# Performance work log

Measured on AMD Instinct MI355X. Metric: run time of the kernel, lower is better.

Reference implementation:

```python
import jax, jax.numpy as jnp
import numpy as np
import math

B, S, DIM, H, HD = 2, 2048, 2048, 16, 128


def _rotary(t, cos, sin):
    # t: [B, S, H, HD]; cos/sin: [S, HD//2]
    tr = t.reshape(*t.shape[:-1], HD // 2, 2)
    t_re, t_im = tr[..., 0], tr[..., 1]
    c = cos[None, :, None, :]
    s = sin[None, :, None, :]
    o_re = t_re * c - t_im * s
    o_im = t_re * s + t_im * c
    out = jnp.stack([o_re, o_im], axis=-1)
    return out.reshape(t.shape)


def setup_inputs() -> dict:
    key = jax.random.key(0)
    ks = jax.random.split(key, 6)
    x = jax.random.normal(ks[0], (B, S, DIM), dtype=jnp.float32)
    # rotary frequencies (base 10000), matching complex freqs_cis = exp(i * t * freq)
    inv_freq = 1.0 / (10000.0 ** (np.arange(0, HD, 2, dtype=np.float32) / HD))
    t = np.arange(S, dtype=np.float32)
    ang = np.outer(t, inv_freq)  # [S, HD//2]
    freqs_cos = jnp.asarray(np.cos(ang), dtype=jnp.float32)
    freqs_sin = jnp.asarray(np.sin(ang), dtype=jnp.float32)
    # causal boolean mask [1,1,S,S]
    mask = jnp.tril(jnp.ones((S, S), dtype=bool))[None, None]
    scale = 0.02
    qw = jax.random.normal(ks[1], (DIM, H * HD), dtype=jnp.float32) * scale
    kw = jax.random.normal(ks[2], (DIM, H * HD), dtype=jnp.float32) * scale
    vw = jax.random.normal(ks[3], (DIM, H * HD), dtype=jnp.float32) * scale
    ow = jax.random.normal(ks[4], (H * HD, DIM), dtype=jnp.float32) * scale
    return {"x": x, "freqs_cos": freqs_cos, "freqs_sin": freqs_sin, "mask": mask,
            "qw": qw, "kw": kw, "vw": vw, "ow": ow}


def reference(x, freqs_cos, freqs_sin, mask, qw, kw, vw, ow):
    bsz, slen, _ = x.shape
    q = (x @ qw).reshape(bsz, slen, H, HD)
    k = (x @ kw).reshape(bsz, slen, H, HD)
    v = (x @ vw).reshape(bsz, slen, H, HD)
    q = _rotary(q, freqs_cos[:slen], freqs_sin[:slen])
    k = _rotary(k, freqs_cos[:slen], freqs_sin[:slen])
    # [B, H, S, HD]
    q = q.transpose(0, 2, 1, 3)
    k = k.transpose(0, 2, 1, 3)
    v = v.transpose(0, 2, 1, 3)
    scale = 1.0 / math.sqrt(HD)
    scores = jnp.einsum('bhqd,bhkd->bhqk', q, k) * scale
    neg_inf = jnp.finfo(scores.dtype).min
    scores = jnp.where(mask, scores, neg_inf)
    attn_w = jax.nn.softmax(scores, axis=-1)
    attn = jnp.einsum('bhqk,bhkd->bhqd', attn_w, v)
    attn = attn.transpose(0, 2, 1, 3).reshape(bsz, slen, H * HD)
    out = attn @ ow
    return (out, attn_w)
```

## Files before the change

kernel.cpp:

```cpp
#include <hip/hip_runtime.h>
#include <stdint.h>

#define S 2048
#define DIMM 2048
#define NH 16
#define HD 128
#define NB 2
#define M4 4096

typedef unsigned short u16;
typedef unsigned int u32;
typedef __attribute__((ext_vector_type(8))) short short8;
typedef __attribute__((ext_vector_type(4))) float f32x4;

__device__ __forceinline__ u16 f2bf(float f) {
  union { float f; u32 u; } v; v.f = f;
  u32 u = v.u + 0x7fffu + ((v.u >> 16) & 1u);
  return (u16)(u >> 16);
}
__device__ __forceinline__ float bf2f(u16 b) {
  union { u32 u; float f; } v; v.u = ((u32)b) << 16;
  return v.f;
}
__device__ __forceinline__ u32 cvt_pk_bf16(float lo, float hi) {
  u32 r; asm("v_cvt_pk_bf16_f32 %0, %1, %2" : "=v"(r) : "v"(lo), "v"(hi)); return r;
}
__device__ __forceinline__ void gl_lds16(const void* g, void* l) {
  __builtin_amdgcn_global_load_lds((const __attribute__((address_space(1))) void*)g,
                                   (__attribute__((address_space(3))) void*)l, 16, 0, 0);
}

__global__ __launch_bounds__(256) void k_conv_x(const float* __restrict__ x, u16* __restrict__ xb) {
  int i = (blockIdx.x * 256 + threadIdx.x) * 8;
  float4 a = *(const float4*)&x[i];
  float4 b = *(const float4*)&x[i + 4];
  uint4 o;
  o.x = (u32)f2bf(a.x) | ((u32)f2bf(a.y) << 16);
  o.y = (u32)f2bf(a.z) | ((u32)f2bf(a.w) << 16);
  o.z = (u32)f2bf(b.x) | ((u32)f2bf(b.y) << 16);
  o.w = (u32)f2bf(b.z) | ((u32)f2bf(b.w) << 16);
  *(uint4*)&xb[i] = o;
}

__global__ __launch_bounds__(256) void k_transpose_w4(const float* __restrict__ w0, const float* __restrict__ w1,
                                                      const float* __restrict__ w2, const float* __restrict__ w3,
                                                      u16* __restrict__ t0, u16* __restrict__ t1,
                                                      u16* __restrict__ t2, u16* __restrict__ t3) {
  __shared__ u16 t[64][72];
  int zi = blockIdx.z;
  const float* w = (zi == 0) ? w0 : (zi == 1) ? w1 : (zi == 2) ? w2 : w3;
  u16* wt = (zi == 0) ? t0 : (zi == 1) ? t1 : (zi == 2) ? t2 : t3;
  int k0 = blockIdx.y * 64, n0 = blockIdx.x * 64;
  int tid = threadIdx.x;
  int r0 = tid >> 4, c4 = (tid & 15) * 4;
#pragma unroll
  for (int p = 0; p < 4; ++p) {
    int r = r0 + p * 16;
    float4 v = *(const float4*)&w[(size_t)(k0 + r) * DIMM + n0 + c4];
    t[c4 + 0][r] = f2bf(v.x); t[c4 + 1][r] = f2bf(v.y);
    t[c4 + 2][r] = f2bf(v.z); t[c4 + 3][r] = f2bf(v.w);
  }
  __syncthreads();
#pragma unroll
  for (int p = 0; p < 2; ++p) {
    int cc = tid + p * 256;
    int rn = cc >> 3, ck = (cc & 7) * 8;
    *(uint4*)&wt[(size_t)(n0 + rn) * DIMM + k0 + ck] = *(const uint4*)&t[rn][ck];
  }
}

__device__ __forceinline__ void gemm128_core(const u16* __restrict__ A, const u16* __restrict__ Bt,
                                             int m0, int n0, int Kd, u16* lA, u16* lB,
                                             f32x4 acc[4][4]) {
  int tid = threadIdx.x;
  int lane = tid & 63;
  int wid = tid >> 6;
  int wm = wid >> 1, wn = wid & 1;
  int c0 = tid, c1 = tid + 256;
  int a_r0 = c0 >> 2, a_k0 = (c0 & 3) * 8;
  int a_r1 = c1 >> 2, a_k1 = (c1 & 3) * 8;
  int ln = lane & 15, sub = lane >> 4;
  for (int kt = 0; kt < Kd; kt += 32) {
    gl_lds16(&A[(size_t)(m0 + a_r0) * Kd + kt + a_k0], &lA[c0 * 8]);
    gl_lds16(&A[(size_t)(m0 + a_r1) * Kd + kt + a_k1], &lA[c1 * 8]);
    gl_lds16(&Bt[(size_t)(n0 + a_r0) * Kd + kt + a_k0], &lB[c0 * 8]);
    gl_lds16(&Bt[(size_t)(n0 + a_r1) * Kd + kt + a_k1], &lB[c1 * 8]);
    __syncthreads();
    short8 af[4], bf[4];
#pragma unroll
    for (int mf = 0; mf < 4; ++mf)
      af[mf] = *(const short8*)&lA[(wm * 64 + mf * 16 + ln) * 32 + sub * 8];
#pragma unroll
    for (int nf = 0; nf < 4; ++nf)
      bf[nf] = *(const short8*)&lB[(wn * 64 + nf * 16 + ln) * 32 + sub * 8];
#pragma unroll
    for (int mf = 0; mf < 4; ++mf)
#pragma unroll
      for (int nf = 0; nf < 4; ++nf)
        acc[mf][nf] = __builtin_amdgcn_mfma_f32_16x16x32_bf16(af[mf], bf[nf], acc[mf][nf], 0, 0, 0);
    __syncthreads();
  }
}

__global__ __launch_bounds__(256) void k_gemm_qkv(const u16* __restrict__ xb,
                                                  const u16* __restrict__ qwT, const u16* __restrict__ kwT,
                                                  const u16* __restrict__ vwT,
                                                  const float* __restrict__ fc, const float* __restrict__ fs,
                                                  u16* __restrict__ qws, u16* __restrict__ kws,
                                                  u16* __restrict__ vtws, float* __restrict__ aw_all) {
  __shared__ u16 lA[128 * 32], lB[128 * 32];
  int f = blockIdx.y * 48 + blockIdx.x;
  int fp = (f & 7) * 192 + (f >> 3);
  int bx = fp % 48, byy = fp / 48;

  {
    int tid = threadIdx.x;
    f32x4 zf = {0.f, 0.f, 0.f, 0.f};
#pragma unroll
    for (int z = 0; z < 5; ++z) {
      int t = f * 5 + z;
      int head = t / 240;
      int r = t - head * 240;
      int qt = 15;
#pragma unroll
      for (int q = 15; q >= 1; --q) {
        if (r >= q * (31 - q)) { qt = q; break; }
        if (q == 1) qt = 0;
      }
      int j = r - qt * (31 - qt);
      int kt = 2 * qt + 2 + j;
      float* base = aw_all + (size_t)head * S * S + (size_t)(qt * 128) * S + kt * 64;
#pragma unroll
      for (int i = 0; i < 8; ++i) {
        int c = i * 256 + tid;
        int row = c >> 4, col = (c & 15) * 4;
        __builtin_nontemporal_store(zf, (f32x4*)&base[(size_t)row * S + col]);
      }
    }
  }

  int region = bx >> 4;
  const u16* Bt = (region == 0) ? qwT : ((region == 1) ? kwT : vwT);
  int n0 = (bx & 15) * 128;
  int m0 = byy * 128;
  f32x4 acc[4][4];
  f32x4 z4 = {0.f, 0.f, 0.f, 0.f};
#pragma unroll
  for (int i = 0; i < 4; ++i)
#pragma unroll
    for (int j = 0; j < 4; ++j) acc[i][j] = z4;
  gemm128_core(xb, Bt, m0, n0, DIMM, lA, lB, acc);
  int lane = threadIdx.x & 63, wid = threadIdx.x >> 6;
  int wm = wid >> 1, wn = wid & 1;
  int ln = lane & 15, sub = lane >> 4;
  if (region == 2) {
#pragma unroll
    for (int mf = 0; mf < 4; ++mf)
#pragma unroll
      for (int nf = 0; nf < 4; ++nf) {
        int m = m0 + wm * 64 + mf * 16 + sub * 4;
        int nl = n0 + wn * 64 + nf * 16 + ln;
        int b = m >> 11, s = m & 2047;
        int h = nl >> 7, d = nl & 127;
        u32 w0 = cvt_pk_bf16(acc[mf][nf][0], acc[mf][nf][1]);
        u32 w1 = cvt_pk_bf16(acc[mf][nf][2], acc[mf][nf][3]);
        uint2 pw = {w0, w1};
        *(uint2*)&vtws[((size_t)((b << 4) + h) * HD + d) * S + s] = pw;
      }
  } else {
    u16* dst = (region == 0) ? qws : kws;
#pragma unroll
    for (int mf = 0; mf < 4; ++mf)
#pragma unroll
      for (int nf = 0; nf < 4; ++nf) {
        int mbase = m0 + wm * 64 + mf * 16 + sub * 4;
        int nl = n0 + wn * 64 + nf * 16 + ln;
        int h = nl >> 7, d = nl & 127;
        int pi = d >> 1;
#pragma unroll
        for (int r = 0; r < 4; ++r) {
          int m = mbase + r;
          int b = m >> 11, s = m & 2047;
          float c = fc[s * 64 + pi];
          float sn = fs[s * 64 + pi];
          float v = acc[mf][nf][r];
          float prt = __shfl_xor(v, 1);
          float o = (ln & 1) ? (prt * sn + v * c) : (v * c - prt * sn);
          float o2 = __shfl_xor(o, 1);
          if (!(ln & 1)) {
            u32 opk = cvt_pk_bf16(o, o2);
            *(u32*)&dst[((size_t)((b << 4) + h) * S + s) * HD + d] = opk;
          }
        }
      }
  }
}

__global__ __launch_bounds__(512, 4) void k_attn(const u16* __restrict__ qws, const u16* __restrict__ kws,
                                                 const u16* __restrict__ vtws,
                                                 float* __restrict__ aw_all, u16* __restrict__ att) {
  __shared__ u16 lK[2][64 * 128];
  __shared__ u16 lV[2][128 * 64];
  __shared__ u16 lP[128 * 64];

  int f = blockIdx.y * 16 + blockIdx.x;
  int x = f & 7;
  int j = f >> 3;
  int by = 4 * x + (j & 3);
  int u = j >> 2;
  int qt = (u < 8) ? u : 23 - u;
  int b = by >> 4, h = by & 15;
  const u16* qb = qws + (size_t)by * S * HD;
  const u16* kb = kws + (size_t)by * S * HD;
  const u16* vb = vtws + (size_t)by * HD * S;
  float* aw = aw_all + (size_t)by * S * S;
  int tid = threadIdx.x, lane = tid & 63, w = tid >> 6;
  int sub = lane >> 4, ln = lane & 15;
  int l7 = ln & 7;
  int q0 = qt * 128;
  int qrow = w * 16 + ln;
  int nkt = 2 * qt + 2;
  const float SC = 0.08838834764831845f * 1.4426950408889634f;

  auto stageK = [&](int kt, int bs) {
#pragma unroll
    for (int i = 0; i < 2; ++i) {
      int c = tid + i * 512;
      int row = c >> 4, p = c & 15;
      gl_lds16(&kb[(size_t)(kt * 64 + row) * HD + ((p ^ (row & 7)) << 3)], &lK[bs][c * 8]);
    }
  };
  auto stageV = [&](int kt, int bs) {
#pragma unroll
    for (int i = 0; i < 2; ++i) {
      int c = tid + i * 512;
      int row = c >> 3, p = c & 7;
      gl_lds16(&vb[(size_t)row * S + kt * 64 + ((p ^ (row & 7)) << 3)], &lV[bs][c * 8]);
    }
  };

  u16* lVlin = &lV[0][0];
#pragma unroll
  for (int i = 0; i < 4; ++i) {
    int c = tid + i * 512;
    int row = c >> 4, p = c & 15;
    gl_lds16(&qb[(size_t)(q0 + row) * HD + ((p ^ (row & 7)) << 3)], &lVlin[c * 8]);
  }
  stageK(0, 0);
  __syncthreads();

  short8 qf[4];
#pragma unroll
  for (int ks = 0; ks < 4; ++ks)
    qf[ks] = *(const short8*)&lVlin[qrow * 128 + (((ks * 4 + sub) ^ l7) << 3)];

  float ts = 0.f;
  for (int kt = 0; kt < nkt; ++kt) {
    int cur = kt & 1;
    if (kt + 1 < nkt) stageK(kt + 1, cur ^ 1);
    f32x4 sacc[4];
    f32x4 z4 = {0.f, 0.f, 0.f, 0.f};
#pragma unroll
    for (int nf = 0; nf < 4; ++nf) sacc[nf] = z4;
    __builtin_amdgcn_s_setprio(1);
#pragma unroll
    for (int nf = 0; nf < 4; ++nf) {
      int krow = nf * 16 + ln;
#pragma unroll
      for (int ks = 0; ks < 4; ++ks) {
        short8 kf = *(const short8*)&lK[cur][krow * 128 + (((ks * 4 + sub) ^ l7) << 3)];
        sacc[nf] = __builtin_amdgcn_mfma_f32_16x16x32_bf16(kf, qf[ks], sacc[nf], 0, 0, 0);
      }
    }
    __builtin_amdgcn_s_setprio(0);
    bool msk = (kt >= 2 * qt);
#pragma unroll
    for (int nf = 0; nf < 4; ++nf)
#pragma unroll
      for (int r = 0; r < 4; ++r) {
        float zz = sacc[nf][r] * SC;
        bool dead = msk && (kt * 64 + nf * 16 + sub * 4 + r > q0 + qrow);
        if (!dead) ts += exp2f(zz);
      }
    __syncthreads();
  }
  ts += __shfl_xor(ts, 16);
  ts += __shfl_xor(ts, 32);
  float mb = __log2f(ts);

  f32x4 oacc[8];
  {
    f32x4 z4 = {0.f, 0.f, 0.f, 0.f};
#pragma unroll
    for (int i = 0; i < 8; ++i) oacc[i] = z4;
  }
  stageK(nkt - 1, 0);
  stageV(nkt - 1, 0);
  __syncthreads();
  for (int it = 0; it < nkt; ++it) {
    int kt = nkt - 1 - it;
    int cur = it & 1;
    if (it + 1 < nkt) { stageK(kt - 1, cur ^ 1); stageV(kt - 1, cur ^ 1); }
    f32x4 sacc[4];
    f32x4 z4 = {0.f, 0.f, 0.f, 0.f};
#pragma unroll
    for (int nf = 0; nf < 4; ++nf) sacc[nf] = z4;
    __builtin_amdgcn_s_setprio(1);
#pragma unroll
    for (int nf = 0; nf < 4; ++nf) {
      int krow = nf * 16 + ln;
#pragma unroll
      for (int ks = 0; ks < 4; ++ks) {
        short8 kf = *(const short8*)&lK[cur][krow * 128 + (((ks * 4 + sub) ^ l7) << 3)];
        sacc[nf] = __builtin_amdgcn_mfma_f32_16x16x32_bf16(kf, qf[ks], sacc[nf], 0, 0, 0);
      }
    }
    __builtin_amdgcn_s_setprio(0);
    bool msk = (kt >= 2 * qt);
#pragma unroll
    for (int nf = 0; nf < 4; ++nf) {
      float p0 = exp2f(sacc[nf][0] * SC - mb);
      float p1 = exp2f(sacc[nf][1] * SC - mb);
      float p2 = exp2f(sacc[nf][2] * SC - mb);
      float p3 = exp2f(sacc[nf][3] * SC - mb);
      if (msk) {
        int base = kt * 64 + nf * 16 + sub * 4 - (q0 + qrow);
        if (base + 0 > 0) p0 = 0.f;
        if (base + 1 > 0) p1 = 0.f;
        if (base + 2 > 0) p2 = 0.f;
        if (base + 3 > 0) p3 = 0.f;
      }
      f32x4 pv = {p0, p1, p2, p3};
      __builtin_nontemporal_store(pv, (f32x4*)&aw[(size_t)(q0 + qrow) * S + kt * 64 + nf * 16 + sub * 4]);
      u32 w0 = cvt_pk_bf16(p0, p1);
      u32 w1 = cvt_pk_bf16(p2, p3);
      uint2 pw = {w0, w1};
      *(uint2*)&lP[qrow * 64 + (((nf * 2 + (sub >> 1)) ^ l7) << 3) + ((sub & 1) << 2)] = pw;
    }
    short8 pa[2];
#pragma unroll
    for (int ks2 = 0; ks2 < 2; ++ks2)
      pa[ks2] = *(const short8*)&lP[qrow * 64 + (((ks2 * 4 + sub) ^ l7) << 3)];
    __builtin_amdgcn_s_setprio(1);
#pragma unroll
    for (int nf2 = 0; nf2 < 8; ++nf2) {
      int drow = nf2 * 16 + ln;
#pragma unroll
      for (int ks2 = 0; ks2 < 2; ++ks2) {
        short8 vv = *(const short8*)&lV[cur][drow * 64 + (((ks2 * 4 + sub) ^ l7) << 3)];
        oacc[nf2] = __builtin_amdgcn_mfma_f32_16x16x32_bf16(vv, pa[ks2], oacc[nf2], 0, 0, 0);
      }
    }
    __builtin_amdgcn_s_setprio(0);
    __syncthreads();
  }

#pragma unroll
  for (int nf2 = 0; nf2 < 8; ++nf2) {
    u32 w0 = cvt_pk_bf16(oacc[nf2][0], oacc[nf2][1]);
    u32 w1 = cvt_pk_bf16(oacc[nf2][2], oacc[nf2][3]);
    uint2 ow2 = {w0, w1};
    *(uint2*)&att[(size_t)(b * S + q0 + qrow) * (NH * HD) + h * 128 + nf2 * 16 + sub * 4] = ow2;
  }
}

__global__ __launch_bounds__(256) void k_gemm_out(const u16* __restrict__ att, const u16* __restrict__ owT,
                                                  float* __restrict__ out) {
  __shared__ u16 lA[128 * 32], lB[128 * 32];
  int f = blockIdx.y * 16 + blockIdx.x;
  int fp = (f & 7) * 64 + (f >> 3);
  int n0 = (fp & 15) * 128, m0 = (fp >> 4) * 128;
  f32x4 acc[4][4];
  f32x4 z4 = {0.f, 0.f, 0.f, 0.f};
#pragma unroll
  for (int i = 0; i < 4; ++i)
#pragma unroll
    for (int j = 0; j < 4; ++j) acc[i][j] = z4;
  gemm128_core(att, owT, m0, n0, DIMM, lA, lB, acc);
  int lane = threadIdx.x & 63, wid = threadIdx.x >> 6;
  int wm = wid >> 1, wn = wid & 1;
  int ln = lane & 15, sub = lane >> 4;
#pragma unroll
  for (int mf = 0; mf < 4; ++mf)
#pragma unroll
    for (int nf = 0; nf < 4; ++nf)
#pragma unroll
      for (int r = 0; r < 4; ++r) {
        int m = m0 + wm * 64 + mf * 16 + sub * 4 + r;
        int nl = n0 + wn * 64 + nf * 16 + ln;
        out[(size_t)m * DIMM + nl] = acc[mf][nf][r];
      }
}

extern "C" void kernel_launch(void* const* d_in, const int* in_sizes, int n_in,
                              void* d_out, int out_size, void* d_ws, size_t ws_size,
                              hipStream_t stream) {
  const float* x  = (const float*)d_in[0];
  const float* fc = (const float*)d_in[1];
  const float* fs = (const float*)d_in[2];
  const float* qw = (const float*)d_in[4];
  const float* kw = (const float*)d_in[5];
  const float* vw = (const float*)d_in[6];
  const float* ow = (const float*)d_in[7];
  float* out = (float*)d_out;
  float* aw  = out + (size_t)M4 * DIMM;

  char* wsb = (char*)d_ws;
  u16* xb   = (u16*)(wsb);
  u16* qwT  = (u16*)(wsb + (size_t)16 * 1024 * 1024);
  u16* kwT  = (u16*)(wsb + (size_t)24 * 1024 * 1024);
  u16* vwT  = (u16*)(wsb + (size_t)32 * 1024 * 1024);
  u16* owT  = (u16*)(wsb + (size_t)40 * 1024 * 1024);
  u16* qws  = (u16*)(wsb + (size_t)48 * 1024 * 1024);
  u16* kws  = (u16*)(wsb + (size_t)64 * 1024 * 1024);
  u16* vtws = (u16*)(wsb + (size_t)80 * 1024 * 1024);
  u16* att  = (u16*)(wsb + (size_t)96 * 1024 * 1024);

  k_conv_x<<<4096, 256, 0, stream>>>(x, xb);
  k_transpose_w4<<<dim3(32, 32, 4), 256, 0, stream>>>(qw, kw, vw, ow, qwT, kwT, vwT, owT);
  k_gemm_qkv<<<dim3(48, 32), 256, 0, stream>>>(xb, qwT, kwT, vwT, fc, fs, qws, kws, vtws, aw);
  k_attn<<<dim3(16, 32), 512, 0, stream>>>(qws, kws, vtws, aw, att);
  k_gemm_out<<<dim3(16, 32), 256, 0, stream>>>(att, owT, out);
}
```

Measured before the change: 419.3 us.

## Rewrite QKV GEMM as 256x256 tile, 8-wave kernel with double-buffered LDS

Replaces the 128x128, 4-wave QKV projection GEMM with a 256x256-tile, 512-thread kernel (384 blocks). K-step is 64, LDS is double-buffered with XOR swizzle, and async global-to-LDS prefetch of the next K-tile is interleaved with MFMA phases using explicit waitcnt and barriers. The aim is more data reuse per LDS load and overlapping memory with compute. It costs heavy register pressure (128 accumulator floats per thread), 128KB of LDS, and a more fragile hand-scheduled sync scheme. Zero-filling of the masked attention weights is redistributed to match the new grid.

```diff
diff --git a/kernel.cpp b/kernel.cpp
--- a/kernel.cpp
+++ b/kernel.cpp
@@ -29,6 +29,7 @@
   __builtin_amdgcn_global_load_lds((const __attribute__((address_space(1))) void*)g,
                                    (__attribute__((address_space(3))) void*)l, 16, 0, 0);
 }
+#define MFMA16(a, b, c) __builtin_amdgcn_mfma_f32_16x16x32_bf16(a, b, c, 0, 0, 0)
 
 __global__ __launch_bounds__(256) void k_conv_x(const float* __restrict__ x, u16* __restrict__ xb) {
   int i = (blockIdx.x * 256 + threadIdx.x) * 8;
@@ -97,28 +98,28 @@
     for (int mf = 0; mf < 4; ++mf)
 #pragma unroll
       for (int nf = 0; nf < 4; ++nf)
-        acc[mf][nf] = __builtin_amdgcn_mfma_f32_16x16x32_bf16(af[mf], bf[nf], acc[mf][nf], 0, 0, 0);
+        acc[mf][nf] = MFMA16(af[mf], bf[nf], acc[mf][nf]);
     __syncthreads();
   }
 }
 
-__global__ __launch_bounds__(256) void k_gemm_qkv(const u16* __restrict__ xb,
-                                                  const u16* __restrict__ qwT, const u16* __restrict__ kwT,
-                                                  const u16* __restrict__ vwT,
-                                                  const float* __restrict__ fc, const float* __restrict__ fs,
-                                                  u16* __restrict__ qws, u16* __restrict__ kws,
-                                                  u16* __restrict__ vtws, float* __restrict__ aw_all) {
-  __shared__ u16 lA[128 * 32], lB[128 * 32];
-  int f = blockIdx.y * 48 + blockIdx.x;
-  int fp = (f & 7) * 192 + (f >> 3);
-  int bx = fp % 48, byy = fp / 48;
+__global__ __launch_bounds__(512, 2) void k_gemm_qkv8(const u16* __restrict__ xb,
+                                                      const u16* __restrict__ qwT, const u16* __restrict__ kwT,
+                                                      const u16* __restrict__ vwT,
+                                                      const float* __restrict__ fc, const float* __restrict__ fs,
+                                                      u16* __restrict__ qws, u16* __restrict__ kws,
+                                                      u16* __restrict__ vtws, float* __restrict__ aw_all) {
+  __shared__ u16 sm[2][2][256 * 64];
+  int tid = threadIdx.x;
+  int f = blockIdx.x;
+  int fp = (f & 7) * 48 + (f >> 3);
+  int bx = fp % 24, by = fp / 24;
 
   {
-    int tid = threadIdx.x;
     f32x4 zf = {0.f, 0.f, 0.f, 0.f};
 #pragma unroll
-    for (int z = 0; z < 5; ++z) {
-      int t = f * 5 + z;
+    for (int z = 0; z < 20; ++z) {
+      int t = f * 20 + z;
       int head = t / 240;
       int r = t - head * 240;
       int qt = 15;
@@ -131,35 +132,150 @@
       int kt = 2 * qt + 2 + j;
       float* base = aw_all + (size_t)head * S * S + (size_t)(qt * 128) * S + kt * 64;
 #pragma unroll
-      for (int i = 0; i < 8; ++i) {
-        int c = i * 256 + tid;
+      for (int i = 0; i < 4; ++i) {
+        int c = i * 512 + tid;
         int row = c >> 4, col = (c & 15) * 4;
         __builtin_nontemporal_store(zf, (f32x4*)&base[(size_t)row * S + col]);
       }
     }
   }
 
-  int region = bx >> 4;
+  int region = bx >> 3;
   const u16* Bt = (region == 0) ? qwT : ((region == 1) ? kwT : vwT);
-  int n0 = (bx & 15) * 128;
-  int m0 = byy * 128;
-  f32x4 acc[4][4];
+  int n0g = (bx & 7) * 256;
+  int m0g = by * 256;
+
+  int lane = tid & 63, wid = tid >> 6;
+  int wm = wid >> 2, wn = wid & 3;
+  int ln = lane & 15, sub = lane >> 4;
+
+  auto stagePart = [&](int t, int bs, int part) {
+    int mat = part >> 1, r0 = (part & 1) << 7;
+    const u16* src = mat ? Bt : xb;
+    int rb = (mat ? n0g : m0g) + r0;
+    int kk = t << 6;
+#pragma unroll
+    for (int i = 0; i < 2; ++i) {
+      int c = tid + i * 512;
+      int row = c >> 3, p = c & 7;
+      gl_lds16(&src[(size_t)(rb + row) * DIMM + kk + ((p ^ (row & 7)) << 3)],
+               &sm[bs][mat][((r0 + row) << 6) + (p << 3)]);
+    }
+  };
+  auto rdA = [&](int bs, int mf, int ks) -> short8 {
+    int row = (wm << 7) + (mf << 4) + ln;
+    return *(const short8*)&sm[bs][0][(row << 6) + ((((ks << 2) + sub) ^ (row & 7)) << 3)];
+  };
+  auto rdB = [&](int bs, int nf, int ks) -> short8 {
+    int row = (wn << 6) + (nf << 4) + ln;
+    return *(const short8*)&sm[bs][1][(row << 6) + ((((ks << 2) + sub) ^ (row & 7)) << 3)];
+  };
+
+  f32x4 acc[8][4];
   f32x4 z4 = {0.f, 0.f, 0.f, 0.f};
 #pragma unroll
-  for (int i = 0; i < 4; ++i)
+  for (int i = 0; i < 8; ++i)
 #pragma unroll
     for (int j = 0; j < 4; ++j) acc[i][j] = z4;
-  gemm128_core(xb, Bt, m0, n0, DIMM, lA, lB, acc);
-  int lane = threadIdx.x & 63, wid = threadIdx.x >> 6;
-  int wm = wid >> 1, wn = wid & 1;
-  int ln = lane & 15, sub = lane >> 4;
+
+  stagePart(0, 0, 0); stagePart(0, 0, 1); stagePart(0, 0, 2); stagePart(0, 0, 3);
+  __syncthreads();
+
+  const int nt = DIMM / 64;
+  for (int t = 0; t < nt; ++t) {
+    int cur = t & 1, nb = cur ^ 1;
+    bool pf = (t + 1 < nt);
+    short8 bfr[4][2];
+    if (pf) { stagePart(t + 1, nb, 0); stagePart(t + 1, nb, 1); }
+    asm volatile("s_waitcnt vmcnt(4)" ::: "memory");
+    __builtin_amdgcn_s_barrier();
+    __builtin_amdgcn_sched_barrier(0);
+#pragma unroll
+    for (int nf = 0; nf < 4; ++nf)
+#pragma unroll
+      for (int ks = 0; ks < 2; ++ks) bfr[nf][ks] = rdB(cur, nf, ks);
+    {
+      short8 a00 = rdA(cur, 0, 0), a01 = rdA(cur, 0, 1);
+      short8 a10 = rdA(cur, 1, 0), a11 = rdA(cur, 1, 1);
+      asm volatile("s_waitcnt lgkmcnt(0)" ::: "memory");
+      __builtin_amdgcn_sched_barrier(0);
+      __builtin_amdgcn_s_setprio(1);
+#pragma unroll
+      for (int nf = 0; nf < 4; ++nf) {
+        acc[0][nf] = MFMA16(a00, bfr[nf][0], acc[0][nf]);
+        acc[0][nf] = MFMA16(a01, bfr[nf][1], acc[0][nf]);
+        acc[1][nf] = MFMA16(a10, bfr[nf][0], acc[1][nf]);
+        acc[1][nf] = MFMA16(a11, bfr[nf][1], acc[1][nf]);
+      }
+      __builtin_amdgcn_s_setprio(0);
+    }
+    __builtin_amdgcn_s_barrier();
+    __builtin_amdgcn_sched_barrier(0);
+    {
+      short8 a00 = rdA(cur, 2, 0), a01 = rdA(cur, 2, 1);
+      short8 a10 = rdA(cur, 3, 0), a11 = rdA(cur, 3, 1);
+      if (pf) { stagePart(t + 1, nb, 2); stagePart(t + 1, nb, 3); }
+      __builtin_amdgcn_s_barrier();
+      asm volatile("s_waitcnt lgkmcnt(0)" ::: "memory");
+      __builtin_amdgcn_sched_barrier(0);
+      __builtin_amdgcn_s_setprio(1);
+#pragma unroll
+      for (int nf = 0; nf < 4; ++nf) {
+        acc[2][nf] = MFMA16(a00, bfr[nf][0], acc[2][nf]);
+        acc[2][nf] = MFMA16(a01, bfr[nf][1], acc[2][nf]);
+        acc[3][nf] = MFMA16(a10, bfr[nf][0], acc[3][nf]);
+        acc[3][nf] = MFMA16(a11, bfr[nf][1], acc[3][nf]);
+      }
+      __builtin_amdgcn_s_setprio(0);
+    }
+    __builtin_amdgcn_s_barrier();
+    __builtin_amdgcn_sched_barrier(0);
+    {
+      short8 a00 = rdA(cur, 4, 0), a01 = rdA(cur, 4, 1);
+      short8 a10 = rdA(cur, 5, 0), a11 = rdA(cur, 5, 1);
+      __builtin_amdgcn_s_barrier();
+      asm volatile("s_waitcnt lgkmcnt(0)" ::: "memory");
+      __builtin_amdgcn_sched_barrier(0);
+      __builtin_amdgcn_s_setprio(1);
+#pragma unroll
+      for (int nf = 0; nf < 4; ++nf) {
+        acc[4][nf] = MFMA16(a00, bfr[nf][0], acc[4][nf]);
+        acc[4][nf] = MFMA16(a01, bfr[nf][1], acc[4][nf]);
+        acc[5][nf] = MFMA16(a10, bfr[nf][0], acc[5][nf]);
+        acc[5][nf] = MFMA16(a11, bfr[nf][1], acc[5][nf]);
+      }
+      __builtin_amdgcn_s_setprio(0);
+    }
+    __builtin_amdgcn_s_barrier();
+    __builtin_amdgcn_sched_barrier(0);
+    {
+      short8 a00 = rdA(cur, 6, 0), a01 = rdA(cur, 6, 1);
+      short8 a10 = rdA(cur, 7, 0), a11 = rdA(cur, 7, 1);
+      __builtin_amdgcn_s_barrier();
+      asm volatile("s_waitcnt lgkmcnt(0)" ::: "memory");
+      __builtin_amdgcn_sched_barrier(0);
+      __builtin_amdgcn_s_setprio(1);
+#pragma unroll
+      for (int nf = 0; nf < 4; ++nf) {
+        acc[6][nf] = MFMA16(a00, bfr[nf][0], acc[6][nf]);
+        acc[6][nf] = MFMA16(a01, bfr[nf][1], acc[6][nf]);
+        acc[7][nf] = MFMA16(a10, bfr[nf][0], acc[7][nf]);
+        acc[7][nf] = MFMA16(a11, bfr[nf][1], acc[7][nf]);
+      }
+      __builtin_amdgcn_s_setprio(0);
+    }
+    asm volatile("s_waitcnt lgkmcnt(0)" ::: "memory");
+    __builtin_amdgcn_s_barrier();
+    __builtin_amdgcn_sched_barrier(0);
+  }
+
   if (region == 2) {
 #pragma unroll
-    for (int mf = 0; mf < 4; ++mf)
+    for (int mf = 0; mf < 8; ++mf)
 #pragma unroll
       for (int nf = 0; nf < 4; ++nf) {
-        int m = m0 + wm * 64 + mf * 16 + sub * 4;
-        int nl = n0 + wn * 64 + nf * 16 + ln;
+        int m = m0g + wm * 128 + mf * 16 + sub * 4;
+        int nl = (bx & 7) * 256 + wn * 64 + nf * 16 + ln;
         int b = m >> 11, s = m & 2047;
         int h = nl >> 7, d = nl & 127;
         u32 w0 = cvt_pk_bf16(acc[mf][nf][0], acc[mf][nf][1]);
@@ -170,11 +286,11 @@
   } else {
     u16* dst = (region == 0) ? qws : kws;
 #pragma unroll
-    for (int mf = 0; mf < 4; ++mf)
+    for (int mf = 0; mf < 8; ++mf)
 #pragma unroll
       for (int nf = 0; nf < 4; ++nf) {
-        int mbase = m0 + wm * 64 + mf * 16 + sub * 4;
-        int nl = n0 + wn * 64 + nf * 16 + ln;
+        int mbase = m0g + wm * 128 + mf * 16 + sub * 4;
+        int nl = (bx & 7) * 256 + wn * 64 + nf * 16 + ln;
         int h = nl >> 7, d = nl & 127;
         int pi = d >> 1;
 #pragma unroll
@@ -269,7 +385,7 @@
 #pragma unroll
       for (int ks = 0; ks < 4; ++ks) {
         short8 kf = *(const short8*)&lK[cur][krow * 128 + (((ks * 4 + sub) ^ l7) << 3)];
-        sacc[nf] = __builtin_amdgcn_mfma_f32_16x16x32_bf16(kf, qf[ks], sacc[nf], 0, 0, 0);
+        sacc[nf] = MFMA16(kf, qf[ks], sacc[nf]);
       }
     }
     __builtin_amdgcn_s_setprio(0);
@@ -289,11 +405,8 @@
   float mb = __log2f(ts);
 
   f32x4 oacc[8];
-  {
-    f32x4 z4 = {0.f, 0.f, 0.f, 0.f};
-#pragma unroll
-    for (int i = 0; i < 8; ++i) oacc[i] = z4;
-  }
+#pragma unroll
+  for (int i = 0; i < 8; ++i) oacc[i] = f32x4{0.f, 0.f, 0.f, 0.f};
   stageK(nkt - 1, 0);
   stageV(nkt - 1, 0);
   __syncthreads();
@@ -302,9 +415,8 @@
     int cur = it & 1;
     if (it + 1 < nkt) { stageK(kt - 1, cur ^ 1); stageV(kt - 1, cur ^ 1); }
     f32x4 sacc[4];
-    f32x4 z4 = {0.f, 0.f, 0.f, 0.f};
-#pragma unroll
-    for (int nf = 0; nf < 4; ++nf) sacc[nf] = z4;
+#pragma unroll
+    for (int nf = 0; nf < 4; ++nf) sacc[nf] = f32x4{0.f, 0.f, 0.f, 0.f};
     __builtin_amdgcn_s_setprio(1);
 #pragma unroll
     for (int nf = 0; nf < 4; ++nf) {
@@ -312,7 +424,7 @@
 #pragma unroll
       for (int ks = 0; ks < 4; ++ks) {
         short8 kf = *(const short8*)&lK[cur][krow * 128 + (((ks * 4 + sub) ^ l7) << 3)];
-        sacc[nf] = __builtin_amdgcn_mfma_f32_16x16x32_bf16(kf, qf[ks], sacc[nf], 0, 0, 0);
+        sacc[nf] = MFMA16(kf, qf[ks], sacc[nf]);
       }
     }
     __builtin_amdgcn_s_setprio(0);
@@ -348,7 +460,7 @@
 #pragma unroll
       for (int ks2 = 0; ks2 < 2; ++ks2) {
         short8 vv = *(const short8*)&lV[cur][drow * 64 + (((ks2 * 4 + sub) ^ l7) << 3)];
-        oacc[nf2] = __builtin_amdgcn_mfma_f32_16x16x32_bf16(vv, pa[ks2], oacc[nf2], 0, 0, 0);
+        oacc[nf2] = MFMA16(vv, pa[ks2], oacc[nf2]);
       }
     }
     __builtin_amdgcn_s_setprio(0);
@@ -418,7 +530,7 @@
 
   k_conv_x<<<4096, 256, 0, stream>>>(x, xb);
   k_transpose_w4<<<dim3(32, 32, 4), 256, 0, stream>>>(qw, kw, vw, ow, qwT, kwT, vwT, owT);
-  k_gemm_qkv<<<dim3(48, 32), 256, 0, stream>>>(xb, qwT, kwT, vwT, fc, fs, qws, kws, vtws, aw);
+  k_gemm_qkv8<<<384, 512, 0, stream>>>(xb, qwT, kwT, vwT, fc, fs, qws, kws, vtws, aw);
   k_attn<<<dim3(16, 32), 512, 0, stream>>>(qws, kws, vtws, aw, att);
   k_gemm_out<<<dim3(16, 32), 256, 0, stream>>>(att, owT, out);
 }
```

Measured after the change: 427.4 us. No clear change (+2.0%).

## Halve attention query tile to 64 rows with 32-key blocks and finer zero-fill

Applied to the files above, without the earlier changes.

The attention kernel now uses 64-query tiles with 256 threads and 32-wide key blocks, launching 1024 blocks with a new interleaved head/q-tile mapping to balance causal work. The QKV GEMM's zero-fill of masked attention-weight regions is re-indexed to 64x64 tiles so the zeroed area follows the finer diagonal. The aim is better load balance, finer causal skipping and more resident blocks per CU. In exchange each block reloads K/V more often per query row, and the masked-tile boundary logic becomes more complex.

```diff
diff --git a/kernel.cpp b/kernel.cpp
--- a/kernel.cpp
+++ b/kernel.cpp
@@ -29,6 +29,7 @@
   __builtin_amdgcn_global_load_lds((const __attribute__((address_space(1))) void*)g,
                                    (__attribute__((address_space(3))) void*)l, 16, 0, 0);
 }
+#define MFMA16(a, b, c) __builtin_amdgcn_mfma_f32_16x16x32_bf16(a, b, c, 0, 0, 0)
 
 __global__ __launch_bounds__(256) void k_conv_x(const float* __restrict__ x, u16* __restrict__ xb) {
   int i = (blockIdx.x * 256 + threadIdx.x) * 8;
@@ -97,7 +98,7 @@
     for (int mf = 0; mf < 4; ++mf)
 #pragma unroll
       for (int nf = 0; nf < 4; ++nf)
-        acc[mf][nf] = __builtin_amdgcn_mfma_f32_16x16x32_bf16(af[mf], bf[nf], acc[mf][nf], 0, 0, 0);
+        acc[mf][nf] = MFMA16(af[mf], bf[nf], acc[mf][nf]);
     __syncthreads();
   }
 }
@@ -117,24 +118,25 @@
     int tid = threadIdx.x;
     f32x4 zf = {0.f, 0.f, 0.f, 0.f};
 #pragma unroll
-    for (int z = 0; z < 5; ++z) {
-      int t = f * 5 + z;
-      int head = t / 240;
-      int r = t - head * 240;
-      int qt = 15;
-#pragma unroll
-      for (int q = 15; q >= 1; --q) {
-        if (r >= q * (31 - q)) { qt = q; break; }
-        if (q == 1) qt = 0;
-      }
-      int j = r - qt * (31 - qt);
-      int kt = 2 * qt + 2 + j;
-      float* base = aw_all + (size_t)head * S * S + (size_t)(qt * 128) * S + kt * 64;
-#pragma unroll
-      for (int i = 0; i < 8; ++i) {
-        int c = i * 256 + tid;
-        int row = c >> 4, col = (c & 15) * 4;
-        __builtin_nontemporal_store(zf, (f32x4*)&base[(size_t)row * S + col]);
+    for (int z = 0; z < 11; ++z) {
+      int t = f * 11 + z;
+      if (t < 15872) {
+        int head = t / 496;
+        int r = t - head * 496;
+        int a = 0;
+#pragma unroll
+        for (int q = 30; q >= 1; --q) {
+          if (r >= q * (63 - q) / 2) { a = q; break; }
+        }
+        int j = r - a * (63 - a) / 2;
+        int kt = a + 1 + j;
+        float* base = aw_all + (size_t)head * S * S + (size_t)(a * 64) * S + kt * 64;
+#pragma unroll
+        for (int i = 0; i < 4; ++i) {
+          int c = i * 256 + tid;
+          int row = c >> 4, col = (c & 15) * 4;
+          __builtin_nontemporal_store(zf, (f32x4*)&base[(size_t)row * S + col]);
+        }
       }
     }
   }
@@ -196,19 +198,21 @@
   }
 }
 
-__global__ __launch_bounds__(512, 4) void k_attn(const u16* __restrict__ qws, const u16* __restrict__ kws,
+__global__ __launch_bounds__(256, 4) void k_attn(const u16* __restrict__ qws, const u16* __restrict__ kws,
                                                  const u16* __restrict__ vtws,
                                                  float* __restrict__ aw_all, u16* __restrict__ att) {
-  __shared__ u16 lK[2][64 * 128];
-  __shared__ u16 lV[2][128 * 64];
-  __shared__ u16 lP[128 * 64];
-
-  int f = blockIdx.y * 16 + blockIdx.x;
+  __shared__ u16 lK[2][32 * 128];
+  __shared__ u16 lV[2][128 * 32];
+  __shared__ u16 lP[64 * 32];
+
+  int f = blockIdx.x;
   int x = f & 7;
   int j = f >> 3;
-  int by = 4 * x + (j & 3);
-  int u = j >> 2;
-  int qt = (u < 8) ? u : 23 - u;
+  int cu = j & 31;
+  int u = j >> 5;
+  int by = 4 * x + u;
+  int c2 = (u & 2) ? ((cu + 16) & 31) : cu;
+  int qt = (u & 1) ? (31 - c2) : c2;
   int b = by >> 4, h = by & 15;
   const u16* qb = qws + (size_t)by * S * HD;
   const u16* kb = kws + (size_t)by * S * HD;
@@ -216,8 +220,8 @@
   float* aw = aw_all + (size_t)by * S * S;
   int tid = threadIdx.x, lane = tid & 63, w = tid >> 6;
   int sub = lane >> 4, ln = lane & 15;
-  int l7 = ln & 7;
-  int q0 = qt * 128;
+  int l7 = ln & 7, l3 = ln & 3;
+  int q0 = qt * 64;
   int qrow = w * 16 + ln;
   int nkt = 2 * qt + 2;
   const float SC = 0.08838834764831845f * 1.4426950408889634f;
@@ -225,24 +229,24 @@
   auto stageK = [&](int kt, int bs) {
 #pragma unroll
     for (int i = 0; i < 2; ++i) {
-      int c = tid + i * 512;
+      int c = tid + i * 256;
       int row = c >> 4, p = c & 15;
-      gl_lds16(&kb[(size_t)(kt * 64 + row) * HD + ((p ^ (row & 7)) << 3)], &lK[bs][c * 8]);
+      gl_lds16(&kb[(size_t)(kt * 32 + row) * HD + ((p ^ (row & 7)) << 3)], &lK[bs][c * 8]);
     }
   };
   auto stageV = [&](int kt, int bs) {
 #pragma unroll
     for (int i = 0; i < 2; ++i) {
-      int c = tid + i * 512;
-      int row = c >> 3, p = c & 7;
-      gl_lds16(&vb[(size_t)row * S + kt * 64 + ((p ^ (row & 7)) << 3)], &lV[bs][c * 8]);
+      int c = tid + i * 256;
+      int row = c >> 2, p = c & 3;
+      gl_lds16(&vb[(size_t)row * S + kt * 32 + ((p ^ (row & 3)) << 3)], &lV[bs][c * 8]);
     }
   };
 
   u16* lVlin = &lV[0][0];
 #pragma unroll
   for (int i = 0; i < 4; ++i) {
-    int c = tid + i * 512;
+    int c = tid + i * 256;
     int row = c >> 4, p = c & 15;
     gl_lds16(&qb[(size_t)(q0 + row) * HD + ((p ^ (row & 7)) << 3)], &lVlin[c * 8]);
   }
@@ -258,28 +262,27 @@
   for (int kt = 0; kt < nkt; ++kt) {
     int cur = kt & 1;
     if (kt + 1 < nkt) stageK(kt + 1, cur ^ 1);
-    f32x4 sacc[4];
-    f32x4 z4 = {0.f, 0.f, 0.f, 0.f};
-#pragma unroll
-    for (int nf = 0; nf < 4; ++nf) sacc[nf] = z4;
+    f32x4 sacc[2];
+#pragma unroll
+    for (int nf = 0; nf < 2; ++nf) sacc[nf] = f32x4{0.f, 0.f, 0.f, 0.f};
     __builtin_amdgcn_s_setprio(1);
 #pragma unroll
-    for (int nf = 0; nf < 4; ++nf) {
+    for (int nf = 0; nf < 2; ++nf) {
       int krow = nf * 16 + ln;
 #pragma unroll
       for (int ks = 0; ks < 4; ++ks) {
         short8 kf = *(const short8*)&lK[cur][krow * 128 + (((ks * 4 + sub) ^ l7) << 3)];
-        sacc[nf] = __builtin_amdgcn_mfma_f32_16x16x32_bf16(kf, qf[ks], sacc[nf], 0, 0, 0);
+        sacc[nf] = MFMA16(kf, qf[ks], sacc[nf]);
       }
     }
     __builtin_amdgcn_s_setprio(0);
     bool msk = (kt >= 2 * qt);
 #pragma unroll
-    for (int nf = 0; nf < 4; ++nf)
+    for (int nf = 0; nf < 2; ++nf)
 #pragma unroll
       for (int r = 0; r < 4; ++r) {
         float zz = sacc[nf][r] * SC;
-        bool dead = msk && (kt * 64 + nf * 16 + sub * 4 + r > q0 + qrow);
+        bool dead = msk && (kt * 32 + nf * 16 + sub * 4 + r > q0 + qrow);
         if (!dead) ts += exp2f(zz);
       }
     __syncthreads();
@@ -289,11 +292,8 @@
   float mb = __log2f(ts);
 
   f32x4 oacc[8];
-  {
-    f32x4 z4 = {0.f, 0.f, 0.f, 0.f};
-#pragma unroll
-    for (int i = 0; i < 8; ++i) oacc[i] = z4;
-  }
+#pragma unroll
+  for (int i = 0; i < 8; ++i) oacc[i] = f32x4{0.f, 0.f, 0.f, 0.f};
   stageK(nkt - 1, 0);
   stageV(nkt - 1, 0);
   __syncthreads();
@@ -301,55 +301,49 @@
     int kt = nkt - 1 - it;
     int cur = it & 1;
     if (it + 1 < nkt) { stageK(kt - 1, cur ^ 1); stageV(kt - 1, cur ^ 1); }
-    f32x4 sacc[4];
-    f32x4 z4 = {0.f, 0.f, 0.f, 0.f};
-#pragma unroll
-    for (int nf = 0; nf < 4; ++nf) sacc[nf] = z4;
+    f32x4 sacc[2];
+#pragma unroll
+    for (int nf = 0; nf < 2; ++nf) sacc[nf] = f32x4{0.f, 0.f, 0.f, 0.f};
     __builtin_amdgcn_s_setprio(1);
 #pragma unroll
-    for (int nf = 0; nf < 4; ++nf) {
+    for (int nf = 0; nf < 2; ++nf) {
       int krow = nf * 16 + ln;
 #pragma unroll
       for (int ks = 0; ks < 4; ++ks) {
         short8 kf = *(const short8*)&lK[cur][krow * 128 + (((ks * 4 + sub) ^ l7) << 3)];
-        sacc[nf] = __builtin_amdgcn_mfma_f32_16x16x32_bf16(kf, qf[ks], sacc[nf], 0, 0, 0);
+        sacc[nf] = MFMA16(kf, qf[ks], sacc[nf]);
       }
     }
     __builtin_amdgcn_s_setprio(0);
     bool msk = (kt >= 2 * qt);
 #pragma unroll
-    for (int nf = 0; nf < 4; ++nf) {
+    for (int nf = 0; nf < 2; ++nf) {
       float p0 = exp2f(sacc[nf][0] * SC - mb);
       float p1 = exp2f(sacc[nf][1] * SC - mb);
       float p2 = exp2f(sacc[nf][2] * SC - mb);
       float p3 = exp2f(sacc[nf][3] * SC - mb);
       if (msk) {
-        int base = kt * 64 + nf * 16 + sub * 4 - (q0 + qrow);
+        int base = kt * 32 + nf * 16 + sub * 4 - (q0 + qrow);
         if (base + 0 > 0) p0 = 0.f;
         if (base + 1 > 0) p1 = 0.f;
         if (base + 2 > 0) p2 = 0.f;
         if (base + 3 > 0) p3 = 0.f;
       }
       f32x4 pv = {p0, p1, p2, p3};
-      __builtin_nontemporal_store(pv, (f32x4*)&aw[(size_t)(q0 + qrow) * S + kt * 64 + nf * 16 + sub * 4]);
+      __builtin_nontemporal_store(pv, (f32x4*)&aw[(size_t)(q0 + qrow) * S + kt * 32 + nf * 16 + sub * 4]);
       u32 w0 = cvt_pk_bf16(p0, p1);
       u32 w1 = cvt_pk_bf16(p2, p3);
       uint2 pw = {w0, w1};
-      *(uint2*)&lP[qrow * 64 + (((nf * 2 + (sub >> 1)) ^ l7) << 3) + ((sub & 1) << 2)] = pw;
-    }
-    short8 pa[2];
-#pragma unroll
-    for (int ks2 = 0; ks2 < 2; ++ks2)
-      pa[ks2] = *(const short8*)&lP[qrow * 64 + (((ks2 * 4 + sub) ^ l7) << 3)];
+      int c16 = (2 * nf + (sub >> 1)) ^ l3;
+      *(uint2*)&lP[qrow * 32 + (c16 << 3) + ((sub & 1) << 2)] = pw;
+    }
+    short8 pa = *(const short8*)&lP[qrow * 32 + ((sub ^ l3) << 3)];
     __builtin_amdgcn_s_setprio(1);
 #pragma unroll
     for (int nf2 = 0; nf2 < 8; ++nf2) {
       int drow = nf2 * 16 + ln;
-#pragma unroll
-      for (int ks2 = 0; ks2 < 2; ++ks2) {
-        short8 vv = *(const short8*)&lV[cur][drow * 64 + (((ks2 * 4 + sub) ^ l7) << 3)];
-        oacc[nf2] = __builtin_amdgcn_mfma_f32_16x16x32_bf16(vv, pa[ks2], oacc[nf2], 0, 0, 0);
-      }
+      short8 vv = *(const short8*)&lV[cur][drow * 32 + ((sub ^ (drow & 3)) << 3)];
+      oacc[nf2] = MFMA16(vv, pa, oacc[nf2]);
     }
     __builtin_amdgcn_s_setprio(0);
     __syncthreads();
@@ -419,6 +413,6 @@
   k_conv_x<<<4096, 256, 0, stream>>>(x, xb);
   k_transpose_w4<<<dim3(32, 32, 4), 256, 0, stream>>>(qw, kw, vw, ow, qwT, kwT, vwT, owT);
   k_gemm_qkv<<<dim3(48, 32), 256, 0, stream>>>(xb, qwT, kwT, vwT, fc, fs, qws, kws, vtws, aw);
-  k_attn<<<dim3(16, 32), 512, 0, stream>>>(qws, kws, vtws, aw, att);
+  k_attn<<<1024, 256, 0, stream>>>(qws, kws, vtws, aw, att);
   k_gemm_out<<<dim3(16, 32), 256, 0, stream>>>(att, owT, out);
 }
```

Result: faster. 392.7 us (-6.3%).
